# Kernel tuning notes

Hardware: AMD Instinct MI355X
Metric: run time of the kernel (lower is better)

## Reference

```python
import jax, jax.numpy as jnp
import numpy as np

BN_EPS = 1e-5
N_NODES, N_EDGES, D_IN, HID = 100000, 1600000, 64, 128


def _bn(x, g, b, m, v):
    # BatchNorm1d in eval mode: running stats
    return (x - m) * jax.lax.rsqrt(v + BN_EPS) * g + b


def _gin_agg(x, edge_index, eps):
    # PyG GINConv aggregation: out[dst] = (1+eps)*x[dst] + sum_{src->dst} x[src]
    src, dst = edge_index[0], edge_index[1]
    s = jax.ops.segment_sum(x[src], dst, num_segments=x.shape[0])
    return (1.0 + eps) * x + s


def setup_inputs() -> dict:
    key = jax.random.key(0)
    ks = jax.random.split(key, 24)
    sc = 0.05
    d = {
        'x': jax.random.normal(ks[0], (N_NODES, D_IN), dtype=jnp.float32),
        'edge_index': jax.random.randint(ks[1], (2, N_EDGES), 0, N_NODES, dtype=jnp.int64),
        'eps1': jnp.zeros((), jnp.float32),
        'W1a': jax.random.normal(ks[2], (D_IN, HID), jnp.float32) * sc,
        'b1a': jnp.zeros((HID,), jnp.float32),
        'W1b': jax.random.normal(ks[3], (HID, HID), jnp.float32) * sc,
        'b1b': jnp.zeros((HID,), jnp.float32),
        'g1': jnp.ones((HID,), jnp.float32), 'be1': jnp.zeros((HID,), jnp.float32),
        'm1': jnp.zeros((HID,), jnp.float32), 'v1': jnp.ones((HID,), jnp.float32),
        'eps2': jnp.zeros((), jnp.float32),
        'W2a': jax.random.normal(ks[4], (HID, HID), jnp.float32) * sc,
        'b2a': jnp.zeros((HID,), jnp.float32),
        'g2': jnp.ones((HID,), jnp.float32), 'be2': jnp.zeros((HID,), jnp.float32),
        'm2': jnp.zeros((HID,), jnp.float32), 'v2': jnp.ones((HID,), jnp.float32),
        'eps3': jnp.zeros((), jnp.float32),
        'W3a': jax.random.normal(ks[5], (HID, HID), jnp.float32) * sc,
        'b3a': jnp.zeros((HID,), jnp.float32),
        'W3b': jax.random.normal(ks[6], (HID, HID), jnp.float32) * sc,
        'b3b': jnp.zeros((HID,), jnp.float32),
        'g3': jnp.ones((HID,), jnp.float32), 'be3': jnp.zeros((HID,), jnp.float32),
        'm3': jnp.zeros((HID,), jnp.float32), 'v3': jnp.ones((HID,), jnp.float32),
        'Wl': jax.random.normal(ks[7], (HID, HID), jnp.float32) * sc,
        'bl': jnp.zeros((HID,), jnp.float32),
        'Wf': jax.random.normal(ks[8], (HID, 1), jnp.float32) * sc,
        'bf': jnp.zeros((1,), jnp.float32),
    }
    return d


def reference(x, edge_index, eps1, W1a, b1a, W1b, b1b, g1, be1, m1, v1,
              eps2, W2a, b2a, g2, be2, m2, v2,
              eps3, W3a, b3a, W3b, b3b, g3, be3, m3, v3,
              Wl, bl, Wf, bf):
    # GINConv 1: agg -> Linear(64,128) ReLU -> Linear(128,128) ReLU -> BN
    h = _gin_agg(x, edge_index, eps1)
    h = jax.nn.relu(h @ W1a + b1a)
    h = jax.nn.relu(h @ W1b + b1b)
    h = _bn(h, g1, be1, m1, v1)
    # GINConv 2: agg -> Linear ReLU -> BN
    h = _gin_agg(h, edge_index, eps2)
    h = jax.nn.relu(h @ W2a + b2a)
    h = _bn(h, g2, be2, m2, v2)
    # GINConv 3: agg -> Linear ReLU -> Linear ReLU -> BN
    h = _gin_agg(h, edge_index, eps3)
    h = jax.nn.relu(h @ W3a + b3a)
    h = jax.nn.relu(h @ W3b + b3b)
    h = _bn(h, g3, be3, m3, v3)
    # head: lin1 + ReLU (dropout identity in eval), fc, squeeze
    h = jax.nn.relu(h @ Wl + bl)
    out = (h @ Wf + bf).squeeze(-1)  # [N]
    return out
```

## Files before the change

kernel.cpp:

```cpp
#include <hip/hip_runtime.h>


constexpr int NN  = 100000;
constexpr int NE  = 1600000;
constexpr int DIN = 64;
constexpr int HID = 128;

constexpr int BSH   = 9;
constexpr int NBUCK = 196;
constexpr int NBLK  = 200;
constexpr int CHUNK = 8000;

typedef __attribute__((ext_vector_type(4))) float f32x4;
typedef __attribute__((ext_vector_type(8))) short bf16x8;
typedef __attribute__((ext_vector_type(8))) unsigned short u16x8;

__device__ __forceinline__ short f2bf(float f) {
    union { float f; unsigned u; } x; x.f = f;
    unsigned r = x.u + 0x7fffu + ((x.u >> 16) & 1u);
    return (short)(r >> 16);
}
__device__ __forceinline__ float bf2f(short s) {
    union { unsigned u; float f; } x; x.u = ((unsigned)(unsigned short)s) << 16;
    return x.f;
}

__global__ __launch_bounds__(256)
void bhist_kernel(const int* __restrict__ eidx, int* __restrict__ bcnt,
                  int* __restrict__ pbase) {
    __shared__ int lh[NBUCK];
    int b = blockIdx.x;
    for (int i = threadIdx.x; i < NBUCK; i += 256) lh[i] = 0;
    __syncthreads();
    int e0 = b * CHUNK;
    for (int i = threadIdx.x; i < CHUNK; i += 256)
        atomicAdd(&lh[eidx[NE + e0 + i] >> BSH], 1);
    __syncthreads();
    for (int i = threadIdx.x; i < NBUCK; i += 256)
        pbase[b * NBUCK + i] = atomicAdd(&bcnt[i], lh[i]);
}

__global__ void bscan_kernel(const int* __restrict__ bcnt, int* __restrict__ bbase,
                             int* __restrict__ offs) {
    __shared__ int lds[256];
    int t = threadIdx.x;
    int v = (t < NBUCK) ? bcnt[t] : 0;
    lds[t] = v; __syncthreads();
    #pragma unroll
    for (int o = 1; o < 256; o <<= 1) {
        int x = (t >= o) ? lds[t - o] : 0;
        __syncthreads();
        lds[t] += x;
        __syncthreads();
    }
    if (t < NBUCK) bbase[t] = lds[t] - v;
    if (t == 0) { bbase[NBUCK] = NE; offs[NN] = NE; }
}

__global__ __launch_bounds__(256)
void part_kernel(const int* __restrict__ eidx, const int* __restrict__ bbase,
                 const int* __restrict__ pbase, int2* __restrict__ tmp) {
    __shared__ int lh[NBUCK], lofs[NBUCK], lcnt[NBUCK], gb[NBUCK];
    __shared__ int sb[256];
    __shared__ int2 lp[CHUNK];
    int b = blockIdx.x;
    int t = threadIdx.x;
    for (int i = t; i < NBUCK; i += 256) { lh[i] = 0; lcnt[i] = 0; }
    __syncthreads();
    int e0 = b * CHUNK;
    for (int i = t; i < CHUNK; i += 256)
        atomicAdd(&lh[eidx[NE + e0 + i] >> BSH], 1);
    __syncthreads();
    {
        int v = (t < NBUCK) ? lh[t] : 0;
        sb[t] = v; __syncthreads();
        #pragma unroll
        for (int o = 1; o < 256; o <<= 1) {
            int x = (t >= o) ? sb[t - o] : 0;
            __syncthreads();
            sb[t] += x;
            __syncthreads();
        }
        if (t < NBUCK) {
            lofs[t] = sb[t] - v;
            gb[t]   = bbase[t] + pbase[b * NBUCK + t];
        }
    }
    __syncthreads();
    for (int i = t; i < CHUNK; i += 256) {
        int s = eidx[e0 + i], d = eidx[NE + e0 + i];
        int bk = d >> BSH;
        int r = atomicAdd(&lcnt[bk], 1);
        lp[lofs[bk] + r] = int2{s, d};
    }
    __syncthreads();
    for (int i = t; i < CHUNK; i += 256) {
        int2 p = lp[i];
        int bk = p.y >> BSH;
        tmp[gb[bk] + (i - lofs[bk])] = p;
    }
}

__global__ __launch_bounds__(512)
void bsort_kernel(const int* __restrict__ bbase, const int2* __restrict__ tmp,
                  int* __restrict__ offs, int* __restrict__ esrc) {
    __shared__ int h[512], lo[512], cnt[512];
    int bk = blockIdx.x;
    int n0 = bk << BSH;
    int lo0 = bbase[bk], hi0 = bbase[bk + 1];
    int t = threadIdx.x;
    h[t] = 0; cnt[t] = 0;
    __syncthreads();
    for (int i = lo0 + t; i < hi0; i += 512)
        atomicAdd(&h[tmp[i].y - n0], 1);
    __syncthreads();
    int v = h[t];
    lo[t] = v; __syncthreads();
    #pragma unroll
    for (int o = 1; o < 512; o <<= 1) {
        int x = (t >= o) ? lo[t - o] : 0;
        __syncthreads();
        lo[t] += x;
        __syncthreads();
    }
    int excl = lo[t] - v;
    __syncthreads();
    lo[t] = excl;
    __syncthreads();
    if (n0 + t < NN) offs[n0 + t] = lo0 + excl;
    for (int i = lo0 + t; i < hi0; i += 512) {
        int2 p = tmp[i];
        int ld = p.y - n0;
        int r = atomicAdd(&cnt[ld], 1);
        esrc[lo0 + lo[ld] + r] = p.x;
    }
}

__global__ void cvt_kernel(const float* __restrict__ x, unsigned short* __restrict__ xb) {
    int i = blockIdx.x * 256 + threadIdx.x;
    if (i >= NN * DIN / 8) return;
    const f32x4* p = (const f32x4*)x + (size_t)i * 2;
    f32x4 v0 = p[0], v1 = p[1];
    u16x8 o;
    #pragma unroll
    for (int j = 0; j < 4; ++j) {
        o[j]     = (unsigned short)f2bf(v0[j]);
        o[j + 4] = (unsigned short)f2bf(v1[j]);
    }
    ((u16x8*)xb)[i] = o;
}

template<int D>
__global__ __launch_bounds__(256)
void aggb_kernel(const float* __restrict__ hf, const unsigned short* __restrict__ hb,
                 const int* __restrict__ offs, const int* __restrict__ esrc,
                 const float* __restrict__ epsp, float* __restrict__ out) {
    constexpr int TPN = D / 8;
    int node = blockIdx.x * (256 / TPN) + threadIdx.x / TPN;
    int f    = threadIdx.x % TPN;
    if (node >= NN) return;
    const u16x8* h8 = (const u16x8*)hb;
    float eps = 1.0f + *epsp;

    const float* hrow = hf + (size_t)node * D + f * 8;
    f32x4 a0 = *(const f32x4*)hrow * eps;
    f32x4 a1 = *(const f32x4*)(hrow + 4) * eps;
    f32x4 b0 = (f32x4)0.f, b1 = (f32x4)0.f;

    union { unsigned u; float fv; } cvt;
    auto acc8 = [&](u16x8 t, f32x4& x0, f32x4& x1) {
        #pragma unroll
        for (int j = 0; j < 4; ++j) { cvt.u = ((unsigned)t[j]) << 16;     x0[j] += cvt.fv; }
        #pragma unroll
        for (int j = 0; j < 4; ++j) { cvt.u = ((unsigned)t[j + 4]) << 16; x1[j] += cvt.fv; }
    };

    int k = offs[node], k1 = offs[node + 1];
    for (; k + 8 <= k1; k += 8) {
        int s0 = esrc[k+0], s1 = esrc[k+1], s2 = esrc[k+2], s3 = esrc[k+3];
        int s4 = esrc[k+4], s5 = esrc[k+5], s6 = esrc[k+6], s7 = esrc[k+7];
        u16x8 t0 = h8[(size_t)s0*TPN+f], t1 = h8[(size_t)s1*TPN+f];
        u16x8 t2 = h8[(size_t)s2*TPN+f], t3 = h8[(size_t)s3*TPN+f];
        u16x8 t4 = h8[(size_t)s4*TPN+f], t5 = h8[(size_t)s5*TPN+f];
        u16x8 t6 = h8[(size_t)s6*TPN+f], t7 = h8[(size_t)s7*TPN+f];
        acc8(t0, a0, a1); acc8(t1, b0, b1); acc8(t2, a0, a1); acc8(t3, b0, b1);
        acc8(t4, a0, a1); acc8(t5, b0, b1); acc8(t6, a0, a1); acc8(t7, b0, b1);
    }
    for (; k + 2 <= k1; k += 2) {
        u16x8 t0 = h8[(size_t)esrc[k]*TPN+f];
        u16x8 t1 = h8[(size_t)esrc[k+1]*TPN+f];
        acc8(t0, a0, a1); acc8(t1, b0, b1);
    }
    if (k < k1) acc8(h8[(size_t)esrc[k]*TPN+f], a0, a1);

    float* orow = out + (size_t)node * D + f * 8;
    *(f32x4*)orow       = a0 + b0;
    *(f32x4*)(orow + 4) = a1 + b1;
}

__global__ void packall_kernel(const float* __restrict__ W1a, const float* __restrict__ W1b,
                               const float* __restrict__ W2a, const float* __restrict__ W3a,
                               const float* __restrict__ W3b, const float* __restrict__ Wl,
                               short* P1a, short* P1b, short* P2a,
                               short* P3a, short* P3b, short* Pl) {
    const float* W; short* P; int K;
    switch (blockIdx.y) {
        case 0: W = W1a; P = P1a; K = 64;  break;
        case 1: W = W1b; P = P1b; K = 128; break;
        case 2: W = W2a; P = P2a; K = 128; break;
        case 3: W = W3a; P = P3a; K = 128; break;
        case 4: W = W3b; P = P3b; K = 128; break;
        default: W = Wl; P = Pl;  K = 128; break;
    }
    int T = (K / 32) * 8 * 64;
    int idx = blockIdx.x * 256 + threadIdx.x;
    if (idx >= T) return;
    int c  = idx >> 9;
    int nt = (idx >> 6) & 7;
    int l  = idx & 63;
    int col   = nt * 16 + (l & 15);
    int kbase = c * 32 + (l >> 4) * 8;
    bf16x8 hi, lo;
    #pragma unroll
    for (int j = 0; j < 8; ++j) {
        float w = W[(kbase + j) * HID + col];
        short h = f2bf(w);
        hi[j] = h;
        lo[j] = f2bf(w - bf2f(h));
    }
    *(bf16x8*)&P[(size_t)idx * 8]       = hi;
    *(bf16x8*)&P[(size_t)(T + idx) * 8] = lo;
}

__global__ __launch_bounds__(512)
void gemm_bn_kernel(const float* __restrict__ A, const short* __restrict__ P,
                    const float* __restrict__ bias,
                    const float* __restrict__ g, const float* __restrict__ be,
                    const float* __restrict__ m, const float* __restrict__ v,
                    float* __restrict__ out, unsigned short* __restrict__ hbout, int M) {
    constexpr int NCH = 4;
    constexpr int T   = NCH * 8 * 64;
    __shared__ short wlds[2 * T * 8];

    const int tid  = threadIdx.x;
    const int wid  = tid >> 6;
    const int lane = tid & 63;

    for (int i = tid; i < 2 * T; i += 512)
        ((bf16x8*)wlds)[i] = ((const bf16x8*)P)[i];
    __syncthreads();

    const int rlo  = lane & 15;
    const int kgrp = lane >> 4;
    const int row  = blockIdx.x * 128 + wid * 16 + rlo;
    const int r    = row < M ? row : M - 1;
    const float* arow = A + (size_t)r * 128 + kgrp * 8;

    f32x4 acc[8];
    #pragma unroll
    for (int i = 0; i < 8; ++i) acc[i] = (f32x4)0.0f;

    #pragma unroll
    for (int c = 0; c < NCH; ++c) {
        f32x4 a0 = *(const f32x4*)(arow + c * 32);
        f32x4 a1 = *(const f32x4*)(arow + c * 32 + 4);
        bf16x8 ah, al;
        #pragma unroll
        for (int j = 0; j < 4; ++j) {
            short h0 = f2bf(a0[j]);
            short h1 = f2bf(a1[j]);
            ah[j]     = h0;
            ah[j + 4] = h1;
            al[j]     = f2bf(a0[j] - bf2f(h0));
            al[j + 4] = f2bf(a1[j] - bf2f(h1));
        }
        #pragma unroll
        for (int nt = 0; nt < 8; ++nt) {
            int fi = ((c * 8) + nt) * 64 + lane;
            bf16x8 wh = *(bf16x8*)&wlds[(size_t)fi * 8];
            bf16x8 wl = *(bf16x8*)&wlds[(size_t)(T + fi) * 8];
            acc[nt] = __builtin_amdgcn_mfma_f32_16x16x32_bf16(ah, wh, acc[nt], 0, 0, 0);
            acc[nt] = __builtin_amdgcn_mfma_f32_16x16x32_bf16(al, wh, acc[nt], 0, 0, 0);
            acc[nt] = __builtin_amdgcn_mfma_f32_16x16x32_bf16(ah, wl, acc[nt], 0, 0, 0);
        }
    }

    #pragma unroll
    for (int nt = 0; nt < 8; ++nt) {
        int col  = nt * 16 + rlo;
        float bb = bias[col];
        float sv = g[col] * rsqrtf(v[col] + 1e-5f);
        float tv = be[col] - m[col] * sv;
        #pragma unroll
        for (int jj = 0; jj < 4; ++jj) {
            int rr = blockIdx.x * 128 + wid * 16 + kgrp * 4 + jj;
            float val = fmaxf(acc[nt][jj] + bb, 0.f) * sv + tv;
            if (rr < M) {
                out[(size_t)rr * 128 + col] = val;
                hbout[(size_t)rr * 128 + col] = (unsigned short)f2bf(val);
            }
        }
    }
}

template<int K1>
__global__ __launch_bounds__(256)
void fused2_kernel(const float* __restrict__ A,
                   const short* __restrict__ P1, const float* __restrict__ bias1,
                   const short* __restrict__ P2, const float* __restrict__ bias2,
                   const float* __restrict__ g, const float* __restrict__ be,
                   const float* __restrict__ m, const float* __restrict__ v,
                   float* __restrict__ out, unsigned short* __restrict__ hbout, int M) {
    constexpr int NCH1 = K1 / 32;
    constexpr int T1   = NCH1 * 8 * 64;
    constexpr int T2   = 4 * 8 * 64;
    constexpr int LDW  = 136;
    __shared__ short h1hi[64 * LDW];
    __shared__ short h1lo[64 * LDW];

    const int tid  = threadIdx.x;
    const int wid  = tid >> 6;
    const int lane = tid & 63;
    const int rlo  = lane & 15;
    const int kgrp = lane >> 4;

    const int row = blockIdx.x * 64 + wid * 16 + rlo;
    const int r   = row < M ? row : M - 1;
    const float* arow = A + (size_t)r * K1 + kgrp * 8;

    const bf16x8* P1v = (const bf16x8*)P1;
    const bf16x8* P2v = (const bf16x8*)P2;

    f32x4 acc[8];
    #pragma unroll
    for (int i = 0; i < 8; ++i) acc[i] = (f32x4)0.0f;

    #pragma unroll
    for (int c = 0; c < NCH1; ++c) {
        f32x4 a0 = *(const f32x4*)(arow + c * 32);
        f32x4 a1 = *(const f32x4*)(arow + c * 32 + 4);
        bf16x8 ah, al;
        #pragma unroll
        for (int j = 0; j < 4; ++j) {
            short h0 = f2bf(a0[j]);
            short h1 = f2bf(a1[j]);
            ah[j]     = h0;
            ah[j + 4] = h1;
            al[j]     = f2bf(a0[j] - bf2f(h0));
            al[j + 4] = f2bf(a1[j] - bf2f(h1));
        }
        #pragma unroll
        for (int nt = 0; nt < 8; ++nt) {
            int fi = ((c * 8) + nt) * 64 + lane;
            bf16x8 wh = P1v[fi];
            bf16x8 wl = P1v[T1 + fi];
            acc[nt] = __builtin_amdgcn_mfma_f32_16x16x32_bf16(ah, wh, acc[nt], 0, 0, 0);
            acc[nt] = __builtin_amdgcn_mfma_f32_16x16x32_bf16(al, wh, acc[nt], 0, 0, 0);
            acc[nt] = __builtin_amdgcn_mfma_f32_16x16x32_bf16(ah, wl, acc[nt], 0, 0, 0);
        }
    }

    #pragma unroll
    for (int nt = 0; nt < 8; ++nt) {
        int col  = nt * 16 + rlo;
        float bb = bias1[col];
        #pragma unroll
        for (int jj = 0; jj < 4; ++jj) {
            int lr = wid * 16 + kgrp * 4 + jj;
            float val = fmaxf(acc[nt][jj] + bb, 0.f);
            short h = f2bf(val);
            h1hi[lr * LDW + col] = h;
            h1lo[lr * LDW + col] = f2bf(val - bf2f(h));
        }
    }
    __syncthreads();

    f32x4 acc2[8];
    #pragma unroll
    for (int i = 0; i < 8; ++i) acc2[i] = (f32x4)0.0f;
    const int lr2 = wid * 16 + rlo;
    #pragma unroll
    for (int c = 0; c < 4; ++c) {
        bf16x8 ah = *(bf16x8*)&h1hi[lr2 * LDW + c * 32 + kgrp * 8];
        bf16x8 al = *(bf16x8*)&h1lo[lr2 * LDW + c * 32 + kgrp * 8];
        #pragma unroll
        for (int nt = 0; nt < 8; ++nt) {
            int fi = ((c * 8) + nt) * 64 + lane;
            bf16x8 wh = P2v[fi];
            bf16x8 wl = P2v[T2 + fi];
            acc2[nt] = __builtin_amdgcn_mfma_f32_16x16x32_bf16(ah, wh, acc2[nt], 0, 0, 0);
            acc2[nt] = __builtin_amdgcn_mfma_f32_16x16x32_bf16(al, wh, acc2[nt], 0, 0, 0);
            acc2[nt] = __builtin_amdgcn_mfma_f32_16x16x32_bf16(ah, wl, acc2[nt], 0, 0, 0);
        }
    }

    #pragma unroll
    for (int nt = 0; nt < 8; ++nt) {
        int col  = nt * 16 + rlo;
        float bb = bias2[col];
        float sv = g[col] * rsqrtf(v[col] + 1e-5f);
        float tv = be[col] - m[col] * sv;
        #pragma unroll
        for (int jj = 0; jj < 4; ++jj) {
            int rr = blockIdx.x * 64 + wid * 16 + kgrp * 4 + jj;
            float val = fmaxf(acc2[nt][jj] + bb, 0.f) * sv + tv;
            if (rr < M) {
                out[(size_t)rr * 128 + col] = val;
                hbout[(size_t)rr * 128 + col] = (unsigned short)f2bf(val);
            }
        }
    }
}

__global__ __launch_bounds__(256)
void fused3_kernel(const float* __restrict__ A,
                   const short* __restrict__ P1, const float* __restrict__ bias1,
                   const short* __restrict__ P2, const float* __restrict__ bias2,
                   const float* __restrict__ g, const float* __restrict__ be,
                   const float* __restrict__ m, const float* __restrict__ v,
                   const short* __restrict__ Pl, const float* __restrict__ bl,
                   const float* __restrict__ Wf, const float* __restrict__ bf,
                   float* __restrict__ out, int M) {
    constexpr int T  = 4 * 8 * 64;
    constexpr int LDW = 136;
    __shared__ short h1hi[64 * LDW];
    __shared__ short h1lo[64 * LDW];

    const int tid  = threadIdx.x;
    const int wid  = tid >> 6;
    const int lane = tid & 63;
    const int rlo  = lane & 15;
    const int kgrp = lane >> 4;

    const int row = blockIdx.x * 64 + wid * 16 + rlo;
    const int r   = row < M ? row : M - 1;
    const float* arow = A + (size_t)r * 128 + kgrp * 8;

    const bf16x8* P1v = (const bf16x8*)P1;
    const bf16x8* P2v = (const bf16x8*)P2;
    const bf16x8* Plv = (const bf16x8*)Pl;

    f32x4 acc[8];
    #pragma unroll
    for (int i = 0; i < 8; ++i) acc[i] = (f32x4)0.0f;
    #pragma unroll
    for (int c = 0; c < 4; ++c) {
        f32x4 a0 = *(const f32x4*)(arow + c * 32);
        f32x4 a1 = *(const f32x4*)(arow + c * 32 + 4);
        bf16x8 ah, al;
        #pragma unroll
        for (int j = 0; j < 4; ++j) {
            short h0 = f2bf(a0[j]);
            short h1 = f2bf(a1[j]);
            ah[j]     = h0;
            ah[j + 4] = h1;
            al[j]     = f2bf(a0[j] - bf2f(h0));
            al[j + 4] = f2bf(a1[j] - bf2f(h1));
        }
        #pragma unroll
        for (int nt = 0; nt < 8; ++nt) {
            int fi = ((c * 8) + nt) * 64 + lane;
            bf16x8 wh = P1v[fi];
            bf16x8 wl = P1v[T + fi];
            acc[nt] = __builtin_amdgcn_mfma_f32_16x16x32_bf16(ah, wh, acc[nt], 0, 0, 0);
            acc[nt] = __builtin_amdgcn_mfma_f32_16x16x32_bf16(al, wh, acc[nt], 0, 0, 0);
            acc[nt] = __builtin_amdgcn_mfma_f32_16x16x32_bf16(ah, wl, acc[nt], 0, 0, 0);
        }
    }
    #pragma unroll
    for (int nt = 0; nt < 8; ++nt) {
        int col  = nt * 16 + rlo;
        float bb = bias1[col];
        #pragma unroll
        for (int jj = 0; jj < 4; ++jj) {
            int lr = wid * 16 + kgrp * 4 + jj;
            float val = fmaxf(acc[nt][jj] + bb, 0.f);
            short h = f2bf(val);
            h1hi[lr * LDW + col] = h;
            h1lo[lr * LDW + col] = f2bf(val - bf2f(h));
        }
    }
    __syncthreads();

    const int lr2 = wid * 16 + rlo;
    bf16x8 ah2[4], al2[4];
    #pragma unroll
    for (int c = 0; c < 4; ++c) {
        ah2[c] = *(bf16x8*)&h1hi[lr2 * LDW + c * 32 + kgrp * 8];
        al2[c] = *(bf16x8*)&h1lo[lr2 * LDW + c * 32 + kgrp * 8];
    }
    __syncthreads();
    f32x4 acc2[8];
    #pragma unroll
    for (int i = 0; i < 8; ++i) acc2[i] = (f32x4)0.0f;
    #pragma unroll
    for (int c = 0; c < 4; ++c) {
        #pragma unroll
        for (int nt = 0; nt < 8; ++nt) {
            int fi = ((c * 8) + nt) * 64 + lane;
            bf16x8 wh = P2v[fi];
            bf16x8 wl = P2v[T + fi];
            acc2[nt] = __builtin_amdgcn_mfma_f32_16x16x32_bf16(ah2[c], wh, acc2[nt], 0, 0, 0);
            acc2[nt] = __builtin_amdgcn_mfma_f32_16x16x32_bf16(al2[c], wh, acc2[nt], 0, 0, 0);
            acc2[nt] = __builtin_amdgcn_mfma_f32_16x16x32_bf16(ah2[c], wl, acc2[nt], 0, 0, 0);
        }
    }
    #pragma unroll
    for (int nt = 0; nt < 8; ++nt) {
        int col  = nt * 16 + rlo;
        float bb = bias2[col];
        float sv = g[col] * rsqrtf(v[col] + 1e-5f);
        float tv = be[col] - m[col] * sv;
        #pragma unroll
        for (int jj = 0; jj < 4; ++jj) {
            int lr = wid * 16 + kgrp * 4 + jj;
            float val = fmaxf(acc2[nt][jj] + bb, 0.f) * sv + tv;
            short h = f2bf(val);
            h1hi[lr * LDW + col] = h;
            h1lo[lr * LDW + col] = f2bf(val - bf2f(h));
        }
    }
    __syncthreads();

    bf16x8 ah3[4], al3[4];
    #pragma unroll
    for (int c = 0; c < 4; ++c) {
        ah3[c] = *(bf16x8*)&h1hi[lr2 * LDW + c * 32 + kgrp * 8];
        al3[c] = *(bf16x8*)&h1lo[lr2 * LDW + c * 32 + kgrp * 8];
    }
    f32x4 acc3[8];
    #pragma unroll
    for (int i = 0; i < 8; ++i) acc3[i] = (f32x4)0.0f;
    #pragma unroll
    for (int c = 0; c < 4; ++c) {
        #pragma unroll
        for (int nt = 0; nt < 8; ++nt) {
            int fi = ((c * 8) + nt) * 64 + lane;
            bf16x8 wh = Plv[fi];
            bf16x8 wl = Plv[T + fi];
            acc3[nt] = __builtin_amdgcn_mfma_f32_16x16x32_bf16(ah3[c], wh, acc3[nt], 0, 0, 0);
            acc3[nt] = __builtin_amdgcn_mfma_f32_16x16x32_bf16(al3[c], wh, acc3[nt], 0, 0, 0);
            acc3[nt] = __builtin_amdgcn_mfma_f32_16x16x32_bf16(ah3[c], wl, acc3[nt], 0, 0, 0);
        }
    }
    float p0 = 0, p1 = 0, p2 = 0, p3 = 0;
    #pragma unroll
    for (int nt = 0; nt < 8; ++nt) {
        int col  = nt * 16 + rlo;
        float bb = bl[col];
        float wv = Wf[col];
        p0 += fmaxf(acc3[nt][0] + bb, 0.f) * wv;
        p1 += fmaxf(acc3[nt][1] + bb, 0.f) * wv;
        p2 += fmaxf(acc3[nt][2] + bb, 0.f) * wv;
        p3 += fmaxf(acc3[nt][3] + bb, 0.f) * wv;
    }
    #pragma unroll
    for (int o = 1; o < 16; o <<= 1) {
        p0 += __shfl_xor(p0, o);
        p1 += __shfl_xor(p1, o);
        p2 += __shfl_xor(p2, o);
        p3 += __shfl_xor(p3, o);
    }
    if (rlo == 0) {
        int rbase = blockIdx.x * 64 + wid * 16 + kgrp * 4;
        float bfv = bf[0];
        if (rbase + 0 < M) out[rbase + 0] = p0 + bfv;
        if (rbase + 1 < M) out[rbase + 1] = p1 + bfv;
        if (rbase + 2 < M) out[rbase + 2] = p2 + bfv;
        if (rbase + 3 < M) out[rbase + 3] = p3 + bfv;
    }
}

extern "C" void kernel_launch(void* const* d_in, const int* in_sizes, int n_in,
                              void* d_out, int out_size, void* d_ws, size_t ws_size,
                              hipStream_t stream) {
    const float* x    = (const float*)d_in[0];
    const int*   eidx = (const int*)d_in[1];
    const float* eps1 = (const float*)d_in[2];
    const float* W1a  = (const float*)d_in[3];
    const float* b1a  = (const float*)d_in[4];
    const float* W1b  = (const float*)d_in[5];
    const float* b1b  = (const float*)d_in[6];
    const float* g1   = (const float*)d_in[7];
    const float* be1  = (const float*)d_in[8];
    const float* m1   = (const float*)d_in[9];
    const float* v1   = (const float*)d_in[10];
    const float* eps2 = (const float*)d_in[11];
    const float* W2a  = (const float*)d_in[12];
    const float* b2a  = (const float*)d_in[13];
    const float* g2   = (const float*)d_in[14];
    const float* be2  = (const float*)d_in[15];
    const float* m2   = (const float*)d_in[16];
    const float* v2   = (const float*)d_in[17];
    const float* eps3 = (const float*)d_in[18];
    const float* W3a  = (const float*)d_in[19];
    const float* b3a  = (const float*)d_in[20];
    const float* W3b  = (const float*)d_in[21];
    const float* b3b  = (const float*)d_in[22];
    const float* g3   = (const float*)d_in[23];
    const float* be3  = (const float*)d_in[24];
    const float* m3   = (const float*)d_in[25];
    const float* v3   = (const float*)d_in[26];
    const float* Wl   = (const float*)d_in[27];
    const float* bl   = (const float*)d_in[28];
    const float* Wf   = (const float*)d_in[29];
    const float* bfp  = (const float*)d_in[30];

    char* ws = (char*)d_ws;
    size_t off = 0;
    auto alloc = [&](size_t bytes) -> void* {
        off = (off + 255) & ~(size_t)255;
        void* p = ws + off;
        off += bytes;
        return p;
    };

    float*          bufA = (float*)alloc((size_t)NN * 128 * 4);
    float*          bufB = (float*)alloc((size_t)NN * 128 * 4);
    unsigned short* hb   = (unsigned short*)alloc((size_t)NN * 128 * 2);
    int*   offs   = (int*)alloc((size_t)(NN + 1) * 4);
    int*   esrc   = (int*)alloc((size_t)NE * 4);
    int*   bcnt   = (int*)alloc((size_t)NBUCK * 4);
    int*   bbase  = (int*)alloc((size_t)(NBUCK + 1) * 4);
    int*   pbase  = (int*)alloc((size_t)NBLK * NBUCK * 4);
    short* P1a    = (short*)alloc((size_t)2 * DIN * HID * 2);
    short* P1b    = (short*)alloc((size_t)2 * HID * HID * 2);
    short* P2a    = (short*)alloc((size_t)2 * HID * HID * 2);
    short* P3a    = (short*)alloc((size_t)2 * HID * HID * 2);
    short* P3b    = (short*)alloc((size_t)2 * HID * HID * 2);
    short* Pl     = (short*)alloc((size_t)2 * HID * HID * 2);
    int2*  tmp    = (int2*)bufA;

    const int GRID_G    = (NN + 127) / 128;
    const int GRID_F    = (NN + 63) / 64;
    const int GRID_A64  = (NN + 31) / 32;
    const int GRID_A128 = (NN + 15) / 16;

    hipMemsetAsync(bcnt, 0, (size_t)NBUCK * 4, stream);
    bhist_kernel<<<NBLK, 256, 0, stream>>>(eidx, bcnt, pbase);
    bscan_kernel<<<1, 256, 0, stream>>>(bcnt, bbase, offs);
    part_kernel<<<NBLK, 256, 0, stream>>>(eidx, bbase, pbase, tmp);
    bsort_kernel<<<NBUCK, 512, 0, stream>>>(bbase, tmp, offs, esrc);

    {
        dim3 grid(8, 6);
        packall_kernel<<<grid, 256, 0, stream>>>(W1a, W1b, W2a, W3a, W3b, Wl,
                                                 P1a, P1b, P2a, P3a, P3b, Pl);
    }
    cvt_kernel<<<(NN * DIN / 8 + 255) / 256, 256, 0, stream>>>(x, hb);

    aggb_kernel<64><<<GRID_A64, 256, 0, stream>>>(x, hb, offs, esrc, eps1, bufA);
    fused2_kernel<64><<<GRID_F, 256, 0, stream>>>(bufA, P1a, b1a, P1b, b1b,
                                                  g1, be1, m1, v1, bufB, hb, NN);
    aggb_kernel<128><<<GRID_A128, 256, 0, stream>>>(bufB, hb, offs, esrc, eps2, bufA);
    gemm_bn_kernel<<<GRID_G, 512, 0, stream>>>(bufA, P2a, b2a, g2, be2, m2, v2,
                                               bufB, hb, NN);
    aggb_kernel<128><<<GRID_A128, 256, 0, stream>>>(bufB, hb, offs, esrc, eps3, bufA);
    fused3_kernel<<<GRID_F, 256, 0, stream>>>(bufA, P3a, b3a, P3b, b3b,
                                              g3, be3, m3, v3, Pl, bl, Wf, bfp,
                                              (float*)d_out, NN);
}
```

Measured before the change: 388.3 us.

## Fuse neighbor aggregation into per-layer MLP kernels via LDS bf16 split planes

Each GIN layer now runs as one kernel: the block gathers neighbor sums for its 64 nodes, writes them as bf16 hi/lo planes into LDS, and feeds those straight into the MFMA stages. The float intermediate buffers and separate aggregation kernels go away, and activations are stored as two bf16 planes (hi and lo) in place of fp32 plus a bf16 copy. This cuts global round trips and kernel launches. In exchange, the gather phase runs inside a GEMM-shaped block with more LDS per block, which may lower occupancy and the latency hiding for the irregular gathers. Some __syncthreads are also replaced with wave-local lgkmcnt fences.

```diff
diff --git a/kernel.cpp b/kernel.cpp
--- a/kernel.cpp
+++ b/kernel.cpp
@@ -5,6 +5,7 @@
 constexpr int NE  = 1600000;
 constexpr int DIN = 64;
 constexpr int HID = 128;
+constexpr int LDW = 136;
 
 constexpr int BSH   = 9;
 constexpr int NBUCK = 196;
@@ -23,6 +24,23 @@
 __device__ __forceinline__ float bf2f(short s) {
     union { unsigned u; float f; } x; x.u = ((unsigned)(unsigned short)s) << 16;
     return x.f;
+}
+__device__ __forceinline__ float bfu(unsigned short s) {
+    union { unsigned u; float f; } x; x.u = ((unsigned)s) << 16;
+    return x.f;
+}
+
+__device__ __forceinline__ void wave_lds_fence() {
+    __builtin_amdgcn_sched_barrier(0);
+    asm volatile("s_waitcnt lgkmcnt(0)" ::: "memory");
+    __builtin_amdgcn_sched_barrier(0);
+}
+
+__device__ __forceinline__ void mfma3(f32x4& acc, bf16x8 ah, bf16x8 al,
+                                      bf16x8 wh, bf16x8 wl) {
+    acc = __builtin_amdgcn_mfma_f32_16x16x32_bf16(ah, wh, acc, 0, 0, 0);
+    acc = __builtin_amdgcn_mfma_f32_16x16x32_bf16(al, wh, acc, 0, 0, 0);
+    acc = __builtin_amdgcn_mfma_f32_16x16x32_bf16(ah, wl, acc, 0, 0, 0);
 }
 
 __global__ __launch_bounds__(256)
@@ -148,54 +166,6 @@
         o[j + 4] = (unsigned short)f2bf(v1[j]);
     }
     ((u16x8*)xb)[i] = o;
-}
-
-template<int D>
-__global__ __launch_bounds__(256)
-void aggb_kernel(const float* __restrict__ hf, const unsigned short* __restrict__ hb,
-                 const int* __restrict__ offs, const int* __restrict__ esrc,
-                 const float* __restrict__ epsp, float* __restrict__ out) {
-    constexpr int TPN = D / 8;
-    int node = blockIdx.x * (256 / TPN) + threadIdx.x / TPN;
-    int f    = threadIdx.x % TPN;
-    if (node >= NN) return;
-    const u16x8* h8 = (const u16x8*)hb;
-    float eps = 1.0f + *epsp;
-
-    const float* hrow = hf + (size_t)node * D + f * 8;
-    f32x4 a0 = *(const f32x4*)hrow * eps;
-    f32x4 a1 = *(const f32x4*)(hrow + 4) * eps;
-    f32x4 b0 = (f32x4)0.f, b1 = (f32x4)0.f;
-
-    union { unsigned u; float fv; } cvt;
-    auto acc8 = [&](u16x8 t, f32x4& x0, f32x4& x1) {
-        #pragma unroll
-        for (int j = 0; j < 4; ++j) { cvt.u = ((unsigned)t[j]) << 16;     x0[j] += cvt.fv; }
-        #pragma unroll
-        for (int j = 0; j < 4; ++j) { cvt.u = ((unsigned)t[j + 4]) << 16; x1[j] += cvt.fv; }
-    };
-
-    int k = offs[node], k1 = offs[node + 1];
-    for (; k + 8 <= k1; k += 8) {
-        int s0 = esrc[k+0], s1 = esrc[k+1], s2 = esrc[k+2], s3 = esrc[k+3];
-        int s4 = esrc[k+4], s5 = esrc[k+5], s6 = esrc[k+6], s7 = esrc[k+7];
-        u16x8 t0 = h8[(size_t)s0*TPN+f], t1 = h8[(size_t)s1*TPN+f];
-        u16x8 t2 = h8[(size_t)s2*TPN+f], t3 = h8[(size_t)s3*TPN+f];
-        u16x8 t4 = h8[(size_t)s4*TPN+f], t5 = h8[(size_t)s5*TPN+f];
-        u16x8 t6 = h8[(size_t)s6*TPN+f], t7 = h8[(size_t)s7*TPN+f];
-        acc8(t0, a0, a1); acc8(t1, b0, b1); acc8(t2, a0, a1); acc8(t3, b0, b1);
-        acc8(t4, a0, a1); acc8(t5, b0, b1); acc8(t6, a0, a1); acc8(t7, b0, b1);
-    }
-    for (; k + 2 <= k1; k += 2) {
-        u16x8 t0 = h8[(size_t)esrc[k]*TPN+f];
-        u16x8 t1 = h8[(size_t)esrc[k+1]*TPN+f];
-        acc8(t0, a0, a1); acc8(t1, b0, b1);
-    }
-    if (k < k1) acc8(h8[(size_t)esrc[k]*TPN+f], a0, a1);
-
-    float* orow = out + (size_t)node * D + f * 8;
-    *(f32x4*)orow       = a0 + b0;
-    *(f32x4*)(orow + 4) = a1 + b1;
 }
 
 __global__ void packall_kernel(const float* __restrict__ W1a, const float* __restrict__ W1b,
@@ -232,327 +202,276 @@
     *(bf16x8*)&P[(size_t)(T + idx) * 8] = lo;
 }
 
-__global__ __launch_bounds__(512)
-void gemm_bn_kernel(const float* __restrict__ A, const short* __restrict__ P,
-                    const float* __restrict__ bias,
-                    const float* __restrict__ g, const float* __restrict__ be,
-                    const float* __restrict__ m, const float* __restrict__ v,
-                    float* __restrict__ out, unsigned short* __restrict__ hbout, int M) {
-    constexpr int NCH = 4;
-    constexpr int T   = NCH * 8 * 64;
-    __shared__ short wlds[2 * T * 8];
-
-    const int tid  = threadIdx.x;
-    const int wid  = tid >> 6;
-    const int lane = tid & 63;
-
-    for (int i = tid; i < 2 * T; i += 512)
-        ((bf16x8*)wlds)[i] = ((const bf16x8*)P)[i];
-    __syncthreads();
-
-    const int rlo  = lane & 15;
-    const int kgrp = lane >> 4;
-    const int row  = blockIdx.x * 128 + wid * 16 + rlo;
-    const int r    = row < M ? row : M - 1;
-    const float* arow = A + (size_t)r * 128 + kgrp * 8;
-
-    f32x4 acc[8];
+template<int D>
+__device__ __forceinline__ void agg_phase(const float* __restrict__ xf,
+                                          const unsigned short* __restrict__ selfh,
+                                          const unsigned short* __restrict__ selfl,
+                                          const unsigned short* __restrict__ gath,
+                                          const int* __restrict__ offs,
+                                          const int* __restrict__ esrc,
+                                          float eps, short* ph, short* pl,
+                                          int blk, int M, int tid) {
+    constexpr int TPN = D / 8;
+    constexpr int NPS = 256 / TPN;
+    const u16x8* g8 = (const u16x8*)gath;
+    #pragma unroll
+    for (int sweep = 0; sweep < 64 / NPS; ++sweep) {
+        int ln = sweep * NPS + tid / TPN;
+        int f  = tid % TPN;
+        int gn = blk * 64 + ln; if (gn >= M) gn = M - 1;
+
+        f32x4 a0, a1;
+        if constexpr (D == 64) {
+            const float* xr = xf + (size_t)gn * D + f * 8;
+            a0 = *(const f32x4*)xr;
+            a1 = *(const f32x4*)(xr + 4);
+        } else {
+            u16x8 sh = ((const u16x8*)selfh)[(size_t)gn * TPN + f];
+            u16x8 sl = ((const u16x8*)selfl)[(size_t)gn * TPN + f];
+            #pragma unroll
+            for (int j = 0; j < 4; ++j) {
+                a0[j] = bfu(sh[j])     + bfu(sl[j]);
+                a1[j] = bfu(sh[j + 4]) + bfu(sl[j + 4]);
+            }
+        }
+        a0 *= eps; a1 *= eps;
+        f32x4 b0 = (f32x4)0.f, b1 = (f32x4)0.f;
+
+        auto acc8 = [&](u16x8 t, f32x4& x0, f32x4& x1) {
+            #pragma unroll
+            for (int j = 0; j < 4; ++j) { x0[j] += bfu(t[j]); x1[j] += bfu(t[j + 4]); }
+        };
+
+        int k = offs[gn], k1 = offs[gn + 1];
+        for (; k + 8 <= k1; k += 8) {
+            int s0 = esrc[k+0], s1 = esrc[k+1], s2 = esrc[k+2], s3 = esrc[k+3];
+            int s4 = esrc[k+4], s5 = esrc[k+5], s6 = esrc[k+6], s7 = esrc[k+7];
+            u16x8 t0 = g8[(size_t)s0*TPN+f], t1 = g8[(size_t)s1*TPN+f];
+            u16x8 t2 = g8[(size_t)s2*TPN+f], t3 = g8[(size_t)s3*TPN+f];
+            u16x8 t4 = g8[(size_t)s4*TPN+f], t5 = g8[(size_t)s5*TPN+f];
+            u16x8 t6 = g8[(size_t)s6*TPN+f], t7 = g8[(size_t)s7*TPN+f];
+            acc8(t0, a0, a1); acc8(t1, b0, b1); acc8(t2, a0, a1); acc8(t3, b0, b1);
+            acc8(t4, a0, a1); acc8(t5, b0, b1); acc8(t6, a0, a1); acc8(t7, b0, b1);
+        }
+        for (; k + 2 <= k1; k += 2) {
+            u16x8 t0 = g8[(size_t)esrc[k]*TPN+f];
+            u16x8 t1 = g8[(size_t)esrc[k+1]*TPN+f];
+            acc8(t0, a0, a1); acc8(t1, b0, b1);
+        }
+        if (k < k1) acc8(g8[(size_t)esrc[k]*TPN+f], a0, a1);
+        a0 += b0; a1 += b1;
+
+        bf16x8 hi, lo;
+        #pragma unroll
+        for (int j = 0; j < 4; ++j) {
+            short h;
+            h = f2bf(a0[j]); hi[j]   = h; lo[j]   = f2bf(a0[j] - bf2f(h));
+            h = f2bf(a1[j]); hi[j+4] = h; lo[j+4] = f2bf(a1[j] - bf2f(h));
+        }
+        *(bf16x8*)&ph[ln * LDW + f * 8] = hi;
+        *(bf16x8*)&pl[ln * LDW + f * 8] = lo;
+    }
+}
+
+template<int NCH>
+__device__ __forceinline__ void stage_from_planes(const short* ph, const short* pl,
+                                                  const bf16x8* Pv,
+                                                  int lr2, int kgrp, int lane,
+                                                  f32x4* acc) {
+    constexpr int T = NCH * 8 * 64;
     #pragma unroll
     for (int i = 0; i < 8; ++i) acc[i] = (f32x4)0.0f;
-
     #pragma unroll
     for (int c = 0; c < NCH; ++c) {
-        f32x4 a0 = *(const f32x4*)(arow + c * 32);
-        f32x4 a1 = *(const f32x4*)(arow + c * 32 + 4);
-        bf16x8 ah, al;
-        #pragma unroll
-        for (int j = 0; j < 4; ++j) {
-            short h0 = f2bf(a0[j]);
-            short h1 = f2bf(a1[j]);
-            ah[j]     = h0;
-            ah[j + 4] = h1;
-            al[j]     = f2bf(a0[j] - bf2f(h0));
-            al[j + 4] = f2bf(a1[j] - bf2f(h1));
-        }
+        bf16x8 ah = *(const bf16x8*)&ph[lr2 * LDW + c * 32 + kgrp * 8];
+        bf16x8 al = *(const bf16x8*)&pl[lr2 * LDW + c * 32 + kgrp * 8];
         #pragma unroll
         for (int nt = 0; nt < 8; ++nt) {
             int fi = ((c * 8) + nt) * 64 + lane;
-            bf16x8 wh = *(bf16x8*)&wlds[(size_t)fi * 8];
-            bf16x8 wl = *(bf16x8*)&wlds[(size_t)(T + fi) * 8];
-            acc[nt] = __builtin_amdgcn_mfma_f32_16x16x32_bf16(ah, wh, acc[nt], 0, 0, 0);
-            acc[nt] = __builtin_amdgcn_mfma_f32_16x16x32_bf16(al, wh, acc[nt], 0, 0, 0);
-            acc[nt] = __builtin_amdgcn_mfma_f32_16x16x32_bf16(ah, wl, acc[nt], 0, 0, 0);
-        }
-    }
-
-    #pragma unroll
-    for (int nt = 0; nt < 8; ++nt) {
-        int col  = nt * 16 + rlo;
-        float bb = bias[col];
-        float sv = g[col] * rsqrtf(v[col] + 1e-5f);
-        float tv = be[col] - m[col] * sv;
-        #pragma unroll
-        for (int jj = 0; jj < 4; ++jj) {
-            int rr = blockIdx.x * 128 + wid * 16 + kgrp * 4 + jj;
-            float val = fmaxf(acc[nt][jj] + bb, 0.f) * sv + tv;
-            if (rr < M) {
-                out[(size_t)rr * 128 + col] = val;
-                hbout[(size_t)rr * 128 + col] = (unsigned short)f2bf(val);
-            }
-        }
-    }
-}
-
-template<int K1>
+            mfma3(acc[nt], ah, al, Pv[fi], Pv[T + fi]);
+        }
+    }
+}
+
 __global__ __launch_bounds__(256)
-void fused2_kernel(const float* __restrict__ A,
-                   const short* __restrict__ P1, const float* __restrict__ bias1,
-                   const short* __restrict__ P2, const float* __restrict__ bias2,
+void layer1_kernel(const float* __restrict__ x, const unsigned short* __restrict__ xbh,
+                   const int* __restrict__ offs, const int* __restrict__ esrc,
+                   const float* __restrict__ epsp,
+                   const short* __restrict__ P1, const float* __restrict__ b1,
+                   const short* __restrict__ P2, const float* __restrict__ b2,
                    const float* __restrict__ g, const float* __restrict__ be,
                    const float* __restrict__ m, const float* __restrict__ v,
-                   float* __restrict__ out, unsigned short* __restrict__ hbout, int M) {
-    constexpr int NCH1 = K1 / 32;
-    constexpr int T1   = NCH1 * 8 * 64;
-    constexpr int T2   = 4 * 8 * 64;
-    constexpr int LDW  = 136;
-    __shared__ short h1hi[64 * LDW];
-    __shared__ short h1lo[64 * LDW];
-
+                   unsigned short* __restrict__ outh, unsigned short* __restrict__ outl,
+                   int M) {
+    __shared__ short ph[64 * LDW];
+    __shared__ short pl[64 * LDW];
     const int tid  = threadIdx.x;
     const int wid  = tid >> 6;
     const int lane = tid & 63;
     const int rlo  = lane & 15;
     const int kgrp = lane >> 4;
 
-    const int row = blockIdx.x * 64 + wid * 16 + rlo;
-    const int r   = row < M ? row : M - 1;
-    const float* arow = A + (size_t)r * K1 + kgrp * 8;
-
-    const bf16x8* P1v = (const bf16x8*)P1;
-    const bf16x8* P2v = (const bf16x8*)P2;
-
+    agg_phase<64>(x, nullptr, nullptr, xbh, offs, esrc, 1.0f + *epsp,
+                  ph, pl, blockIdx.x, M, tid);
+    __syncthreads();
+
+    const int lr2 = wid * 16 + rlo;
     f32x4 acc[8];
-    #pragma unroll
-    for (int i = 0; i < 8; ++i) acc[i] = (f32x4)0.0f;
-
-    #pragma unroll
-    for (int c = 0; c < NCH1; ++c) {
-        f32x4 a0 = *(const f32x4*)(arow + c * 32);
-        f32x4 a1 = *(const f32x4*)(arow + c * 32 + 4);
-        bf16x8 ah, al;
-        #pragma unroll
-        for (int j = 0; j < 4; ++j) {
-            short h0 = f2bf(a0[j]);
-            short h1 = f2bf(a1[j]);
-            ah[j]     = h0;
-            ah[j + 4] = h1;
-            al[j]     = f2bf(a0[j] - bf2f(h0));
-            al[j + 4] = f2bf(a1[j] - bf2f(h1));
-        }
-        #pragma unroll
-        for (int nt = 0; nt < 8; ++nt) {
-            int fi = ((c * 8) + nt) * 64 + lane;
-            bf16x8 wh = P1v[fi];
-            bf16x8 wl = P1v[T1 + fi];
-            acc[nt] = __builtin_amdgcn_mfma_f32_16x16x32_bf16(ah, wh, acc[nt], 0, 0, 0);
-            acc[nt] = __builtin_amdgcn_mfma_f32_16x16x32_bf16(al, wh, acc[nt], 0, 0, 0);
-            acc[nt] = __builtin_amdgcn_mfma_f32_16x16x32_bf16(ah, wl, acc[nt], 0, 0, 0);
-        }
-    }
-
+    stage_from_planes<2>(ph, pl, (const bf16x8*)P1, lr2, kgrp, lane, acc);
+    wave_lds_fence();
     #pragma unroll
     for (int nt = 0; nt < 8; ++nt) {
         int col  = nt * 16 + rlo;
-        float bb = bias1[col];
+        float bb = b1[col];
         #pragma unroll
         for (int jj = 0; jj < 4; ++jj) {
             int lr = wid * 16 + kgrp * 4 + jj;
             float val = fmaxf(acc[nt][jj] + bb, 0.f);
             short h = f2bf(val);
-            h1hi[lr * LDW + col] = h;
-            h1lo[lr * LDW + col] = f2bf(val - bf2f(h));
-        }
-    }
-    __syncthreads();
-
-    f32x4 acc2[8];
-    #pragma unroll
-    for (int i = 0; i < 8; ++i) acc2[i] = (f32x4)0.0f;
-    const int lr2 = wid * 16 + rlo;
-    #pragma unroll
-    for (int c = 0; c < 4; ++c) {
-        bf16x8 ah = *(bf16x8*)&h1hi[lr2 * LDW + c * 32 + kgrp * 8];
-        bf16x8 al = *(bf16x8*)&h1lo[lr2 * LDW + c * 32 + kgrp * 8];
-        #pragma unroll
-        for (int nt = 0; nt < 8; ++nt) {
-            int fi = ((c * 8) + nt) * 64 + lane;
-            bf16x8 wh = P2v[fi];
-            bf16x8 wl = P2v[T2 + fi];
-            acc2[nt] = __builtin_amdgcn_mfma_f32_16x16x32_bf16(ah, wh, acc2[nt], 0, 0, 0);
-            acc2[nt] = __builtin_amdgcn_mfma_f32_16x16x32_bf16(al, wh, acc2[nt], 0, 0, 0);
-            acc2[nt] = __builtin_amdgcn_mfma_f32_16x16x32_bf16(ah, wl, acc2[nt], 0, 0, 0);
-        }
-    }
-
+            ph[lr * LDW + col] = h;
+            pl[lr * LDW + col] = f2bf(val - bf2f(h));
+        }
+    }
+    wave_lds_fence();
+
+    stage_from_planes<4>(ph, pl, (const bf16x8*)P2, lr2, kgrp, lane, acc);
     #pragma unroll
     for (int nt = 0; nt < 8; ++nt) {
         int col  = nt * 16 + rlo;
-        float bb = bias2[col];
+        float bb = b2[col];
         float sv = g[col] * rsqrtf(v[col] + 1e-5f);
         float tv = be[col] - m[col] * sv;
         #pragma unroll
         for (int jj = 0; jj < 4; ++jj) {
             int rr = blockIdx.x * 64 + wid * 16 + kgrp * 4 + jj;
-            float val = fmaxf(acc2[nt][jj] + bb, 0.f) * sv + tv;
             if (rr < M) {
-                out[(size_t)rr * 128 + col] = val;
-                hbout[(size_t)rr * 128 + col] = (unsigned short)f2bf(val);
+                float val = fmaxf(acc[nt][jj] + bb, 0.f) * sv + tv;
+                short h = f2bf(val);
+                outh[(size_t)rr * 128 + col] = (unsigned short)h;
+                outl[(size_t)rr * 128 + col] = (unsigned short)f2bf(val - bf2f(h));
             }
         }
     }
 }
 
 __global__ __launch_bounds__(256)
-void fused3_kernel(const float* __restrict__ A,
-                   const short* __restrict__ P1, const float* __restrict__ bias1,
-                   const short* __restrict__ P2, const float* __restrict__ bias2,
+void layer2_kernel(const unsigned short* __restrict__ inh,
+                   const unsigned short* __restrict__ inl,
+                   const int* __restrict__ offs, const int* __restrict__ esrc,
+                   const float* __restrict__ epsp,
+                   const short* __restrict__ P1, const float* __restrict__ b1,
+                   const float* __restrict__ g, const float* __restrict__ be,
+                   const float* __restrict__ m, const float* __restrict__ v,
+                   unsigned short* __restrict__ outh, unsigned short* __restrict__ outl,
+                   int M) {
+    __shared__ short ph[64 * LDW];
+    __shared__ short pl[64 * LDW];
+    const int tid  = threadIdx.x;
+    const int wid  = tid >> 6;
+    const int lane = tid & 63;
+    const int rlo  = lane & 15;
+    const int kgrp = lane >> 4;
+
+    agg_phase<128>(nullptr, inh, inl, inh, offs, esrc, 1.0f + *epsp,
+                   ph, pl, blockIdx.x, M, tid);
+    __syncthreads();
+
+    const int lr2 = wid * 16 + rlo;
+    f32x4 acc[8];
+    stage_from_planes<4>(ph, pl, (const bf16x8*)P1, lr2, kgrp, lane, acc);
+    #pragma unroll
+    for (int nt = 0; nt < 8; ++nt) {
+        int col  = nt * 16 + rlo;
+        float bb = b1[col];
+        float sv = g[col] * rsqrtf(v[col] + 1e-5f);
+        float tv = be[col] - m[col] * sv;
+        #pragma unroll
+        for (int jj = 0; jj < 4; ++jj) {
+            int rr = blockIdx.x * 64 + wid * 16 + kgrp * 4 + jj;
+            if (rr < M) {
+                float val = fmaxf(acc[nt][jj] + bb, 0.f) * sv + tv;
+                short h = f2bf(val);
+                outh[(size_t)rr * 128 + col] = (unsigned short)h;
+                outl[(size_t)rr * 128 + col] = (unsigned short)f2bf(val - bf2f(h));
+            }
+        }
+    }
+}
+
+__global__ __launch_bounds__(256)
+void layer3_kernel(const unsigned short* __restrict__ inh,
+                   const unsigned short* __restrict__ inl,
+                   const int* __restrict__ offs, const int* __restrict__ esrc,
+                   const float* __restrict__ epsp,
+                   const short* __restrict__ P1, const float* __restrict__ b1,
+                   const short* __restrict__ P2, const float* __restrict__ b2,
                    const float* __restrict__ g, const float* __restrict__ be,
                    const float* __restrict__ m, const float* __restrict__ v,
                    const short* __restrict__ Pl, const float* __restrict__ bl,
                    const float* __restrict__ Wf, const float* __restrict__ bf,
                    float* __restrict__ out, int M) {
-    constexpr int T  = 4 * 8 * 64;
-    constexpr int LDW = 136;
-    __shared__ short h1hi[64 * LDW];
-    __shared__ short h1lo[64 * LDW];
-
+    __shared__ short ph[64 * LDW];
+    __shared__ short pl[64 * LDW];
     const int tid  = threadIdx.x;
     const int wid  = tid >> 6;
     const int lane = tid & 63;
     const int rlo  = lane & 15;
     const int kgrp = lane >> 4;
 
-    const int row = blockIdx.x * 64 + wid * 16 + rlo;
-    const int r   = row < M ? row : M - 1;
-    const float* arow = A + (size_t)r * 128 + kgrp * 8;
-
-    const bf16x8* P1v = (const bf16x8*)P1;
-    const bf16x8* P2v = (const bf16x8*)P2;
-    const bf16x8* Plv = (const bf16x8*)Pl;
-
+    agg_phase<128>(nullptr, inh, inl, inh, offs, esrc, 1.0f + *epsp,
+                   ph, pl, blockIdx.x, M, tid);
+    __syncthreads();
+
+    const int lr2 = wid * 16 + rlo;
     f32x4 acc[8];
-    #pragma unroll
-    for (int i = 0; i < 8; ++i) acc[i] = (f32x4)0.0f;
-    #pragma unroll
-    for (int c = 0; c < 4; ++c) {
-        f32x4 a0 = *(const f32x4*)(arow + c * 32);
-        f32x4 a1 = *(const f32x4*)(arow + c * 32 + 4);
-        bf16x8 ah, al;
-        #pragma unroll
-        for (int j = 0; j < 4; ++j) {
-            short h0 = f2bf(a0[j]);
-            short h1 = f2bf(a1[j]);
-            ah[j]     = h0;
-            ah[j + 4] = h1;
-            al[j]     = f2bf(a0[j] - bf2f(h0));
-            al[j + 4] = f2bf(a1[j] - bf2f(h1));
-        }
-        #pragma unroll
-        for (int nt = 0; nt < 8; ++nt) {
-            int fi = ((c * 8) + nt) * 64 + lane;
-            bf16x8 wh = P1v[fi];
-            bf16x8 wl = P1v[T + fi];
-            acc[nt] = __builtin_amdgcn_mfma_f32_16x16x32_bf16(ah, wh, acc[nt], 0, 0, 0);
-            acc[nt] = __builtin_amdgcn_mfma_f32_16x16x32_bf16(al, wh, acc[nt], 0, 0, 0);
-            acc[nt] = __builtin_amdgcn_mfma_f32_16x16x32_bf16(ah, wl, acc[nt], 0, 0, 0);
-        }
-    }
+
+    stage_from_planes<4>(ph, pl, (const bf16x8*)P1, lr2, kgrp, lane, acc);
+    wave_lds_fence();
     #pragma unroll
     for (int nt = 0; nt < 8; ++nt) {
         int col  = nt * 16 + rlo;
-        float bb = bias1[col];
+        float bb = b1[col];
         #pragma unroll
         for (int jj = 0; jj < 4; ++jj) {
             int lr = wid * 16 + kgrp * 4 + jj;
             float val = fmaxf(acc[nt][jj] + bb, 0.f);
             short h = f2bf(val);
-            h1hi[lr * LDW + col] = h;
-            h1lo[lr * LDW + col] = f2bf(val - bf2f(h));
-        }
-    }
-    __syncthreads();
-
-    const int lr2 = wid * 16 + rlo;
-    bf16x8 ah2[4], al2[4];
-    #pragma unroll
-    for (int c = 0; c < 4; ++c) {
-        ah2[c] = *(bf16x8*)&h1hi[lr2 * LDW + c * 32 + kgrp * 8];
-        al2[c] = *(bf16x8*)&h1lo[lr2 * LDW + c * 32 + kgrp * 8];
-    }
-    __syncthreads();
-    f32x4 acc2[8];
-    #pragma unroll
-    for (int i = 0; i < 8; ++i) acc2[i] = (f32x4)0.0f;
-    #pragma unroll
-    for (int c = 0; c < 4; ++c) {
-        #pragma unroll
-        for (int nt = 0; nt < 8; ++nt) {
-            int fi = ((c * 8) + nt) * 64 + lane;
-            bf16x8 wh = P2v[fi];
-            bf16x8 wl = P2v[T + fi];
-            acc2[nt] = __builtin_amdgcn_mfma_f32_16x16x32_bf16(ah2[c], wh, acc2[nt], 0, 0, 0);
-            acc2[nt] = __builtin_amdgcn_mfma_f32_16x16x32_bf16(al2[c], wh, acc2[nt], 0, 0, 0);
-            acc2[nt] = __builtin_amdgcn_mfma_f32_16x16x32_bf16(ah2[c], wl, acc2[nt], 0, 0, 0);
-        }
-    }
+            ph[lr * LDW + col] = h;
+            pl[lr * LDW + col] = f2bf(val - bf2f(h));
+        }
+    }
+    wave_lds_fence();
+
+    stage_from_planes<4>(ph, pl, (const bf16x8*)P2, lr2, kgrp, lane, acc);
+    wave_lds_fence();
     #pragma unroll
     for (int nt = 0; nt < 8; ++nt) {
         int col  = nt * 16 + rlo;
-        float bb = bias2[col];
+        float bb = b2[col];
         float sv = g[col] * rsqrtf(v[col] + 1e-5f);
         float tv = be[col] - m[col] * sv;
         #pragma unroll
         for (int jj = 0; jj < 4; ++jj) {
             int lr = wid * 16 + kgrp * 4 + jj;
-            float val = fmaxf(acc2[nt][jj] + bb, 0.f) * sv + tv;
+            float val = fmaxf(acc[nt][jj] + bb, 0.f) * sv + tv;
             short h = f2bf(val);
-            h1hi[lr * LDW + col] = h;
-            h1lo[lr * LDW + col] = f2bf(val - bf2f(h));
-        }
-    }
-    __syncthreads();
-
-    bf16x8 ah3[4], al3[4];
-    #pragma unroll
-    for (int c = 0; c < 4; ++c) {
-        ah3[c] = *(bf16x8*)&h1hi[lr2 * LDW + c * 32 + kgrp * 8];
-        al3[c] = *(bf16x8*)&h1lo[lr2 * LDW + c * 32 + kgrp * 8];
-    }
-    f32x4 acc3[8];
-    #pragma unroll
-    for (int i = 0; i < 8; ++i) acc3[i] = (f32x4)0.0f;
-    #pragma unroll
-    for (int c = 0; c < 4; ++c) {
-        #pragma unroll
-        for (int nt = 0; nt < 8; ++nt) {
-            int fi = ((c * 8) + nt) * 64 + lane;
-            bf16x8 wh = Plv[fi];
-            bf16x8 wl = Plv[T + fi];
-            acc3[nt] = __builtin_amdgcn_mfma_f32_16x16x32_bf16(ah3[c], wh, acc3[nt], 0, 0, 0);
-            acc3[nt] = __builtin_amdgcn_mfma_f32_16x16x32_bf16(al3[c], wh, acc3[nt], 0, 0, 0);
-            acc3[nt] = __builtin_amdgcn_mfma_f32_16x16x32_bf16(ah3[c], wl, acc3[nt], 0, 0, 0);
-        }
-    }
+            ph[lr * LDW + col] = h;
+            pl[lr * LDW + col] = f2bf(val - bf2f(h));
+        }
+    }
+    wave_lds_fence();
+
+    stage_from_planes<4>(ph, pl, (const bf16x8*)Pl, lr2, kgrp, lane, acc);
     float p0 = 0, p1 = 0, p2 = 0, p3 = 0;
     #pragma unroll
     for (int nt = 0; nt < 8; ++nt) {
         int col  = nt * 16 + rlo;
         float bb = bl[col];
         float wv = Wf[col];
-        p0 += fmaxf(acc3[nt][0] + bb, 0.f) * wv;
-        p1 += fmaxf(acc3[nt][1] + bb, 0.f) * wv;
-        p2 += fmaxf(acc3[nt][2] + bb, 0.f) * wv;
-        p3 += fmaxf(acc3[nt][3] + bb, 0.f) * wv;
+        p0 += fmaxf(acc[nt][0] + bb, 0.f) * wv;
+        p1 += fmaxf(acc[nt][1] + bb, 0.f) * wv;
+        p2 += fmaxf(acc[nt][2] + bb, 0.f) * wv;
+        p3 += fmaxf(acc[nt][3] + bb, 0.f) * wv;
     }
     #pragma unroll
     for (int o = 1; o < 16; o <<= 1) {
@@ -615,9 +534,11 @@
         return p;
     };
 
-    float*          bufA = (float*)alloc((size_t)NN * 128 * 4);
-    float*          bufB = (float*)alloc((size_t)NN * 128 * 4);
-    unsigned short* hb   = (unsigned short*)alloc((size_t)NN * 128 * 2);
+    unsigned short* xbh = (unsigned short*)alloc((size_t)NN * DIN * 2);
+    unsigned short* hAh = (unsigned short*)alloc((size_t)NN * HID * 2);
+    unsigned short* hAl = (unsigned short*)alloc((size_t)NN * HID * 2);
+    unsigned short* hBh = (unsigned short*)alloc((size_t)NN * HID * 2);
+    unsigned short* hBl = (unsigned short*)alloc((size_t)NN * HID * 2);
     int*   offs   = (int*)alloc((size_t)(NN + 1) * 4);
     int*   esrc   = (int*)alloc((size_t)NE * 4);
     int*   bcnt   = (int*)alloc((size_t)NBUCK * 4);
@@ -629,12 +550,9 @@
     short* P3a    = (short*)alloc((size_t)2 * HID * HID * 2);
     short* P3b    = (short*)alloc((size_t)2 * HID * HID * 2);
     short* Pl     = (short*)alloc((size_t)2 * HID * HID * 2);
-    int2*  tmp    = (int2*)bufA;
-
-    const int GRID_G    = (NN + 127) / 128;
-    const int GRID_F    = (NN + 63) / 64;
-    const int GRID_A64  = (NN + 31) / 32;
-    const int GRID_A128 = (NN + 15) / 16;
+    int2*  tmp    = (int2*)hAh;
+
+    const int GRID_F = (NN + 63) / 64;
 
     hipMemsetAsync(bcnt, 0, (size_t)NBUCK * 4, stream);
     bhist_kernel<<<NBLK, 256, 0, stream>>>(eidx, bcnt, pbase);
@@ -647,16 +565,16 @@
         packall_kernel<<<grid, 256, 0, stream>>>(W1a, W1b, W2a, W3a, W3b, Wl,
                                                  P1a, P1b, P2a, P3a, P3b, Pl);
     }
-    cvt_kernel<<<(NN * DIN / 8 + 255) / 256, 256, 0, stream>>>(x, hb);
-
-    aggb_kernel<64><<<GRID_A64, 256, 0, stream>>>(x, hb, offs, esrc, eps1, bufA);
-    fused2_kernel<64><<<GRID_F, 256, 0, stream>>>(bufA, P1a, b1a, P1b, b1b,
-                                                  g1, be1, m1, v1, bufB, hb, NN);
-    aggb_kernel<128><<<GRID_A128, 256, 0, stream>>>(bufB, hb, offs, esrc, eps2, bufA);
-    gemm_bn_kernel<<<GRID_G, 512, 0, stream>>>(bufA, P2a, b2a, g2, be2, m2, v2,
-                                               bufB, hb, NN);
-    aggb_kernel<128><<<GRID_A128, 256, 0, stream>>>(bufB, hb, offs, esrc, eps3, bufA);
-    fused3_kernel<<<GRID_F, 256, 0, stream>>>(bufA, P3a, b3a, P3b, b3b,
+    cvt_kernel<<<(NN * DIN / 8 + 255) / 256, 256, 0, stream>>>(x, xbh);
+
+    layer1_kernel<<<GRID_F, 256, 0, stream>>>(x, xbh, offs, esrc, eps1,
+                                              P1a, b1a, P1b, b1b,
+                                              g1, be1, m1, v1, hAh, hAl, NN);
+    layer2_kernel<<<GRID_F, 256, 0, stream>>>(hAh, hAl, offs, esrc, eps2,
+                                              P2a, b2a, g2, be2, m2, v2,
+                                              hBh, hBl, NN);
+    layer3_kernel<<<GRID_F, 256, 0, stream>>>(hBh, hBl, offs, esrc, eps3,
+                                              P3a, b3a, P3b, b3b,
                                               g3, be3, m3, v3, Pl, bl, Wf, bfp,
                                               (float*)d_out, NN);
 }
```

New measurement: 404.1 us. +4.1%, slower.
